# Kernel optimization log

Hardware: AMD Instinct MI355X
Metric: run time of the kernel (lower is better)

## Reference

```python
import jax, jax.numpy as jnp
import numpy as np

N = 50000       # nodes
E = 800000      # edges (before self loops)
F_IN = 128
NUM_CLASSES = 40
NEG_SLOPE = 0.2


def _glorot(key, shape):
    lim = jnp.sqrt(6.0 / (shape[0] + shape[1]))
    return jax.random.uniform(key, shape, jnp.float32, -lim, lim)


def setup_inputs() -> dict:
    key = jax.random.key(0)
    ks = jax.random.split(key, 32)
    inp = {}
    inp['x'] = jax.random.normal(ks[0], (N, F_IN), jnp.float32)
    inp['edge_index'] = jax.random.randint(ks[1], (2, E), 0, N, dtype=jnp.int32)
    dims = [(F_IN, 128), (128, 128), (128, 256)]
    k = 2
    for i, (din, dout) in enumerate(dims, start=1):
        inp[f'w{i}l'] = _glorot(ks[k], (din, dout)); k += 1
        inp[f'b{i}l'] = jnp.zeros((dout,), jnp.float32)
        inp[f'w{i}r'] = _glorot(ks[k], (din, dout)); k += 1
        inp[f'b{i}r'] = jnp.zeros((dout,), jnp.float32)
        inp[f'a{i}'] = _glorot(ks[k], (dout, 1))[:, 0]; k += 1
        inp[f'o{i}'] = jnp.zeros((dout,), jnp.float32)
    inp['wc'] = _glorot(ks[k], (256, NUM_CLASSES)); k += 1
    inp['bc'] = jnp.zeros((NUM_CLASSES,), jnp.float32)
    return inp


def gatv2_layer(x, src, dst, wl, bl, wr, br, att, bias, n):
    # GATv2 (heads=1): e_ij = att . leaky_relu(Wl x_j + Wr x_i); softmax over j per dst i
    xl = x @ wl + bl                     # [N, dout] (source transform)
    xr = x @ wr + br                     # [N, dout] (target transform)
    h = jax.nn.leaky_relu(xl[src] + xr[dst], NEG_SLOPE)   # [E, dout]
    e = h @ att                          # [E]
    m = jax.ops.segment_max(e, dst, num_segments=n)       # per-dst max (stable softmax)
    p = jnp.exp(e - m[dst])
    s = jax.ops.segment_sum(p, dst, num_segments=n)
    alpha = p / s[dst]                   # [E]
    out = jax.ops.segment_sum(alpha[:, None] * xl[src], dst, num_segments=n)
    return out + bias


def reference(x, edge_index,
              w1l, b1l, w1r, b1r, a1, o1,
              w2l, b2l, w2r, b2r, a2, o2,
              w3l, b3l, w3r, b3r, a3, o3,
              wc, bc):
    n = x.shape[0]
    loops = jnp.arange(n, dtype=edge_index.dtype)
    src = jnp.concatenate([edge_index[0], loops])   # add_self_loops=True (PyG default)
    dst = jnp.concatenate([edge_index[1], loops])
    h = gatv2_layer(x, src, dst, w1l, b1l, w1r, b1r, a1, o1, n)
    h = jax.nn.relu(h)                                # dropout inactive (eval mode)
    h = gatv2_layer(h, src, dst, w2l, b2l, w2r, b2r, a2, o2, n)
    h = jax.nn.relu(h)
    h = gatv2_layer(h, src, dst, w3l, b3l, w3r, b3r, a3, o3, n)
    return h @ wc + bc                                # [N, NUM_CLASSES]
```

## Files before the change

kernel.cpp:

```cpp
#include <hip/hip_runtime.h>
#include <math.h>
#include <stdint.h>


typedef __attribute__((ext_vector_type(8))) short bf16x8;
typedef __attribute__((ext_vector_type(4))) float f32x4;
typedef __attribute__((ext_vector_type(4))) _Float16 half4;
typedef __attribute__((ext_vector_type(2))) _Float16 half2v;
typedef unsigned short ushort_t;

__device__ inline ushort_t bf16_rne(float f) {
  unsigned u = __float_as_uint(f);
  unsigned r = (u + 0x7FFFu + ((u >> 16) & 1u)) >> 16;
  return (ushort_t)r;
}
__device__ inline float bf16_to_f(ushort_t h) {
  return __uint_as_float(((unsigned)h) << 16);
}

__device__ inline float fdot2f(half2v a, half2v b, float c) {
#if __has_builtin(__builtin_amdgcn_fdot2)
  return __builtin_amdgcn_fdot2(a, b, c, false);
#else
  return c + (float)a[0] * (float)b[0] + (float)a[1] * (float)b[1];
#endif
}
__device__ inline half2v h2max(half2v a, half2v b) {
#if __has_builtin(__builtin_elementwise_max)
  return __builtin_elementwise_max(a, b);
#else
  half2v r;
  r[0] = a[0] > b[0] ? a[0] : b[0];
  r[1] = a[1] > b[1] ? a[1] : b[1];
  return r;
#endif
}

__global__ void zero_int_kernel(int* __restrict__ p, int n) {
  int i = blockIdx.x * blockDim.x + threadIdx.x;
  if (i < n) p[i] = 0;
}

__global__ void deg_count_kernel(const int* __restrict__ dst, int E, int n,
                                 int* __restrict__ deg) {
  int i = blockIdx.x * blockDim.x + threadIdx.x;
  int tot = E + n;
  if (i < tot) {
    int d = (i < E) ? dst[i] : (i - E);
    atomicAdd(&deg[d], 1);
  }
}

__global__ __launch_bounds__(256) void block_sum_kernel(
    const int* __restrict__ deg, int n, int* __restrict__ partial) {
  __shared__ int sm[256];
  int base = blockIdx.x * 1024;
  int t = threadIdx.x;
  int sum = 0;
#pragma unroll
  for (int k = 0; k < 4; ++k) {
    int i = base + k * 256 + t;
    sum += (i < n) ? deg[i] : 0;
  }
  sm[t] = sum;
  __syncthreads();
  for (int off = 128; off > 0; off >>= 1) {
    if (t < off) sm[t] += sm[t + off];
    __syncthreads();
  }
  if (t == 0) partial[blockIdx.x] = sm[0];
}

__global__ void scan_partial_kernel(int* __restrict__ partial, int nchunks) {
  int lane = threadIdx.x;
  int v = (lane < nchunks) ? partial[lane] : 0;
#pragma unroll
  for (int off = 1; off < 64; off <<= 1) {
    int u = __shfl_up(v, off, 64);
    if (lane >= off) v += u;
  }
  int ex = __shfl_up(v, 1, 64);
  if (lane == 0) ex = 0;
  if (lane < nchunks) partial[lane] = ex;
}

__global__ __launch_bounds__(1024) void block_scan_kernel(
    const int* __restrict__ deg, const int* __restrict__ partial,
    int* __restrict__ row_ptr, int* __restrict__ cursor, int n) {
  __shared__ int sm[1024];
  int i = blockIdx.x * 1024 + threadIdx.x;
  int v = (i < n) ? deg[i] : 0;
  sm[threadIdx.x] = v;
  __syncthreads();
  for (int off = 1; off < 1024; off <<= 1) {
    int t = (threadIdx.x >= off) ? sm[threadIdx.x - off] : 0;
    __syncthreads();
    sm[threadIdx.x] += t;
    __syncthreads();
  }
  int excl = partial[blockIdx.x] + sm[threadIdx.x] - v;
  if (i < n) {
    row_ptr[i] = excl;
    cursor[i] = excl;
  }
  if (i == n - 1) row_ptr[n] = excl + v;
}

__global__ void scatter_kernel(const int* __restrict__ src,
                               const int* __restrict__ dst, int E, int n,
                               int* __restrict__ cursor,
                               int* __restrict__ col_src) {
  int i = blockIdx.x * blockDim.x + threadIdx.x;
  int tot = E + n;
  if (i < tot) {
    int s = (i < E) ? src[i] : (i - E);
    int d = (i < E) ? dst[i] : (i - E);
    int slot = atomicAdd(&cursor[d], 1);
    col_src[slot] = s;
  }
}

struct PackArgs {
  const float* w[7];
  ushort_t* hi[7];
  ushort_t* lo[7];
  int ntiles[7];
  int kslices[7];
  int N[7];
};

__global__ __launch_bounds__(256) void pack_w_kernel(PackArgs a) {
  int m = blockIdx.y;
  int ntiles = a.ntiles[m];
  int N = a.N[m];
  int tot = a.kslices[m] * ntiles * 512;
  int idx = blockIdx.x * 256 + threadIdx.x;
  if (idx >= tot) return;
  int i = idx & 7;
  int lane = (idx >> 3) & 63;
  int t = (idx >> 9) % ntiles;
  int ks = idx / (512 * ntiles);
  int k = ks * 32 + (lane >> 4) * 8 + i;
  int c = t * 16 + (lane & 15);
  float f = (c < N) ? a.w[m][k * N + c] : 0.f;
  ushort_t h = bf16_rne(f);
  a.hi[m][idx] = h;
  a.lo[m][idx] = bf16_rne(f - bf16_to_f(h));
}

__global__ __launch_bounds__(256) void gemm_dual_mfma(
    const float* __restrict__ X, const ushort_t* __restrict__ wlhi,
    const ushort_t* __restrict__ wllo, const ushort_t* __restrict__ wrhi,
    const ushort_t* __restrict__ wrlo, const float* __restrict__ Bl,
    const float* __restrict__ Br, _Float16* __restrict__ Yl,
    _Float16* __restrict__ Yr, int M, int N, int ntot) {
  int lane = threadIdx.x & 63;
  int wv = threadIdx.x >> 6;
  int kg = lane >> 4;
  int li = lane & 15;
  int rbase = blockIdx.x * 64 + wv * 16;
  int colofs = blockIdx.y * 128;
  int tbase = colofs >> 4;
  int arow = rbase + li;
  int ar = (arow < M) ? arow : (M - 1);
  const float* xp = X + (size_t)ar * 128 + kg * 8;

  f32x4 accl[8], accr[8];
#pragma unroll
  for (int t = 0; t < 8; ++t) {
    accl[t] = (f32x4){0.f, 0.f, 0.f, 0.f};
    accr[t] = (f32x4){0.f, 0.f, 0.f, 0.f};
  }

#pragma unroll
  for (int ks = 0; ks < 4; ++ks) {
    float4 a0 = *reinterpret_cast<const float4*>(xp + ks * 32);
    float4 a1 = *reinterpret_cast<const float4*>(xp + ks * 32 + 4);
    float av[8] = {a0.x, a0.y, a0.z, a0.w, a1.x, a1.y, a1.z, a1.w};
    bf16x8 ah, al;
#pragma unroll
    for (int i = 0; i < 8; ++i) {
      ushort_t h = bf16_rne(av[i]);
      ah[i] = (short)h;
      al[i] = (short)bf16_rne(av[i] - bf16_to_f(h));
    }
    size_t fb = ((size_t)ks * ntot + tbase) * 512 + (size_t)lane * 8;
#pragma unroll
    for (int t = 0; t < 8; ++t) {
      size_t o = fb + (size_t)t * 512;
      bf16x8 blh = *reinterpret_cast<const bf16x8*>(wlhi + o);
      bf16x8 bll = *reinterpret_cast<const bf16x8*>(wllo + o);
      bf16x8 brh = *reinterpret_cast<const bf16x8*>(wrhi + o);
      bf16x8 brl = *reinterpret_cast<const bf16x8*>(wrlo + o);
      accl[t] = __builtin_amdgcn_mfma_f32_16x16x32_bf16(ah, blh, accl[t], 0, 0, 0);
      accl[t] = __builtin_amdgcn_mfma_f32_16x16x32_bf16(ah, bll, accl[t], 0, 0, 0);
      accl[t] = __builtin_amdgcn_mfma_f32_16x16x32_bf16(al, blh, accl[t], 0, 0, 0);
      accr[t] = __builtin_amdgcn_mfma_f32_16x16x32_bf16(ah, brh, accr[t], 0, 0, 0);
      accr[t] = __builtin_amdgcn_mfma_f32_16x16x32_bf16(ah, brl, accr[t], 0, 0, 0);
      accr[t] = __builtin_amdgcn_mfma_f32_16x16x32_bf16(al, brh, accr[t], 0, 0, 0);
    }
  }
  int srow = rbase + kg * 4;
#pragma unroll
  for (int t = 0; t < 8; ++t) {
    int col = colofs + t * 16 + li;
    float bl = Bl[col];
    float br = Br[col];
#pragma unroll
    for (int r = 0; r < 4; ++r) {
      int rr = srow + r;
      if (rr < M) {
        Yl[(size_t)rr * N + col] = (_Float16)(accl[t][r] + bl);
        Yr[(size_t)rr * N + col] = (_Float16)(accr[t][r] + br);
      }
    }
  }
}

__global__ __launch_bounds__(256) void classifier_mfma(
    const float* __restrict__ H, const ushort_t* __restrict__ wchi,
    const ushort_t* __restrict__ wclo, const float* __restrict__ BC,
    float* __restrict__ out, int M) {
  int lane = threadIdx.x & 63;
  int wv = threadIdx.x >> 6;
  int kg = lane >> 4;
  int li = lane & 15;
  int rbase = blockIdx.x * 64 + wv * 16;
  int arow = rbase + li;
  int ar = (arow < M) ? arow : (M - 1);
  const float* xp = H + (size_t)ar * 256 + kg * 8;

  f32x4 acc[3];
#pragma unroll
  for (int t = 0; t < 3; ++t) acc[t] = (f32x4){0.f, 0.f, 0.f, 0.f};

#pragma unroll
  for (int ks = 0; ks < 8; ++ks) {
    float4 a0 = *reinterpret_cast<const float4*>(xp + ks * 32);
    float4 a1 = *reinterpret_cast<const float4*>(xp + ks * 32 + 4);
    float av[8] = {a0.x, a0.y, a0.z, a0.w, a1.x, a1.y, a1.z, a1.w};
    bf16x8 ah, al;
#pragma unroll
    for (int i = 0; i < 8; ++i) {
      ushort_t h = bf16_rne(av[i]);
      ah[i] = (short)h;
      al[i] = (short)bf16_rne(av[i] - bf16_to_f(h));
    }
    size_t fb = ((size_t)ks * 3) * 512 + (size_t)lane * 8;
#pragma unroll
    for (int t = 0; t < 3; ++t) {
      size_t o = fb + (size_t)t * 512;
      bf16x8 bh = *reinterpret_cast<const bf16x8*>(wchi + o);
      bf16x8 bl = *reinterpret_cast<const bf16x8*>(wclo + o);
      acc[t] = __builtin_amdgcn_mfma_f32_16x16x32_bf16(ah, bh, acc[t], 0, 0, 0);
      acc[t] = __builtin_amdgcn_mfma_f32_16x16x32_bf16(ah, bl, acc[t], 0, 0, 0);
      acc[t] = __builtin_amdgcn_mfma_f32_16x16x32_bf16(al, bh, acc[t], 0, 0, 0);
    }
  }
  int srow = rbase + kg * 4;
#pragma unroll
  for (int t = 0; t < 3; ++t) {
    int col = t * 16 + li;
    if (col < 40) {
      float b = BC[col];
#pragma unroll
      for (int r = 0; r < 4; ++r) {
        int rr = srow + r;
        if (rr < M) out[(size_t)rr * 40 + col] = acc[t][r] + b;
      }
    }
  }
}

#define NEG_BIG (-1e30f)
template <int DOUT, bool RELU>
__global__ __launch_bounds__(256) void attn_kernel(
    const _Float16* __restrict__ xl, const _Float16* __restrict__ xr,
    const float* __restrict__ att, const float* __restrict__ bias,
    const int* __restrict__ row_ptr, const int* __restrict__ col_src,
    float* __restrict__ out, int M) {
  constexpr int NQ = DOUT / 64;
  constexpr int NE = NQ * 4;
  int wid = (int)((blockIdx.x * blockDim.x + threadIdx.x) >> 6);
  int lane = threadIdx.x & 63;
  int grp = lane >> 4;
  int sl = lane & 15;
  if (wid >= M) return;

  half2v xr2[NQ * 2], att2[NQ * 2];
  {
    const half4* xrp =
        reinterpret_cast<const half4*>(xr) + (size_t)wid * (DOUT / 4) + sl;
#pragma unroll
    for (int q = 0; q < NQ; ++q) {
      half4 r4 = xrp[q * 16];
      half2v lo, hi;
      lo[0] = r4[0]; lo[1] = r4[1];
      hi[0] = r4[2]; hi[1] = r4[3];
      xr2[q * 2] = lo;
      xr2[q * 2 + 1] = hi;
    }
#pragma unroll
    for (int q = 0; q < NQ; ++q) {
#pragma unroll
      for (int t = 0; t < 2; ++t) {
        int c = q * 64 + sl * 4 + t * 2;
        half2v a2;
        a2[0] = (_Float16)att[c];
        a2[1] = (_Float16)att[c + 1];
        att2[q * 2 + t] = a2;
      }
    }
  }
  half2v v02;
  v02[0] = (_Float16)0.2f;
  v02[1] = (_Float16)0.2f;

  float acc[NE];
#pragma unroll
  for (int i = 0; i < NE; ++i) acc[i] = 0.f;
  float m = NEG_BIG, s = 0.f;
  int e0 = row_ptr[wid], e1 = row_ptr[wid + 1];
  int j = e0 + grp;

  const half4* base = reinterpret_cast<const half4*>(xl);
  half4 xv[NQ], xn[NQ], x2[NQ];
  half4 hz;
  hz[0] = hz[1] = hz[2] = hz[3] = (_Float16)0.f;
#pragma unroll
  for (int q = 0; q < NQ; ++q) {
    xv[q] = hz;
    xn[q] = hz;
    x2[q] = hz;
  }
  if (j < e1) {
    const half4* rp = base + (size_t)col_src[j] * (DOUT / 4) + sl;
#pragma unroll
    for (int q = 0; q < NQ; ++q) xv[q] = rp[q * 16];
  }
  if (j + 4 < e1) {
    const half4* rp = base + (size_t)col_src[j + 4] * (DOUT / 4) + sl;
#pragma unroll
    for (int q = 0; q < NQ; ++q) xn[q] = rp[q * 16];
  }
  int i2 = (j + 8 < e1) ? col_src[j + 8] : 0;

  while (j < e1) {
    int i3 = (j + 12 < e1) ? col_src[j + 12] : 0;
    if (j + 8 < e1) {
      const half4* rp = base + (size_t)i2 * (DOUT / 4) + sl;
#pragma unroll
      for (int q = 0; q < NQ; ++q) x2[q] = rp[q * 16];
    }
    float p = 0.f;
    float xf[NE];
#pragma unroll
    for (int q = 0; q < NQ; ++q) {
#pragma unroll
      for (int t = 0; t < 2; ++t) {
        half2v xa;
        xa[0] = xv[q][2 * t];
        xa[1] = xv[q][2 * t + 1];
        half2v tt = xa + xr2[q * 2 + t];
        tt = h2max(tt, tt * v02);
        p = fdot2f(tt, att2[q * 2 + t], p);
        xf[q * 4 + 2 * t] = (float)xa[0];
        xf[q * 4 + 2 * t + 1] = (float)xa[1];
      }
    }
#pragma unroll
    for (int off = 1; off < 16; off <<= 1) p += __shfl_xor(p, off, 64);
    if (p > m + 8.0f) {
      float sc = __expf(m - p);
      s = s * sc + 1.f;
#pragma unroll
      for (int i = 0; i < NE; ++i) acc[i] = fmaf(acc[i], sc, xf[i]);
      m = p;
    } else {
      float pe = __expf(p - m);
      s += pe;
#pragma unroll
      for (int i = 0; i < NE; ++i) acc[i] = fmaf(pe, xf[i], acc[i]);
    }
#pragma unroll
    for (int q = 0; q < NQ; ++q) {
      xv[q] = xn[q];
      xn[q] = x2[q];
    }
    i2 = i3;
    j += 4;
  }
  float mg = m;
  float mm = m, ss = s;
#pragma unroll
  for (int off = 16; off < 64; off <<= 1) {
    float mo = __shfl_xor(mm, off, 64);
    float so = __shfl_xor(ss, off, 64);
    float nm = fmaxf(mm, mo);
    ss = ss * __expf(mm - nm) + so * __expf(mo - nm);
    mm = nm;
  }
  float scale = __expf(mg - mm) / ss;
#pragma unroll
  for (int i = 0; i < NE; ++i) {
    float v = acc[i] * scale;
#pragma unroll
    for (int off = 16; off < 64; off <<= 1) v += __shfl_xor(v, off, 64);
    acc[i] = v;
  }
#pragma unroll
  for (int q = 0; q < NQ; ++q) {
    if (grp == (q & 3)) {
      int c = q * 64 + sl * 4;
      float4 b4 = *reinterpret_cast<const float4*>(bias + c);
      float4 o;
      o.x = acc[q * 4 + 0] + b4.x;
      o.y = acc[q * 4 + 1] + b4.y;
      o.z = acc[q * 4 + 2] + b4.z;
      o.w = acc[q * 4 + 3] + b4.w;
      if (RELU) {
        o.x = fmaxf(o.x, 0.f); o.y = fmaxf(o.y, 0.f);
        o.z = fmaxf(o.z, 0.f); o.w = fmaxf(o.w, 0.f);
      }
      *reinterpret_cast<float4*>(out + (size_t)wid * DOUT + c) = o;
    }
  }
}

extern "C" void kernel_launch(void* const* d_in, const int* in_sizes, int n_in,
                              void* d_out, int out_size, void* d_ws,
                              size_t ws_size, hipStream_t stream) {
  const float* x = (const float*)d_in[0];
  const int* ei = (const int*)d_in[1];
  const float* w1l = (const float*)d_in[2];
  const float* b1l = (const float*)d_in[3];
  const float* w1r = (const float*)d_in[4];
  const float* b1r = (const float*)d_in[5];
  const float* a1 = (const float*)d_in[6];
  const float* o1 = (const float*)d_in[7];
  const float* w2l = (const float*)d_in[8];
  const float* b2l = (const float*)d_in[9];
  const float* w2r = (const float*)d_in[10];
  const float* b2r = (const float*)d_in[11];
  const float* a2 = (const float*)d_in[12];
  const float* o2 = (const float*)d_in[13];
  const float* w3l = (const float*)d_in[14];
  const float* b3l = (const float*)d_in[15];
  const float* w3r = (const float*)d_in[16];
  const float* b3r = (const float*)d_in[17];
  const float* a3 = (const float*)d_in[18];
  const float* o3 = (const float*)d_in[19];
  const float* wc = (const float*)d_in[20];
  const float* bc = (const float*)d_in[21];
  float* out = (float*)d_out;

  const int n = in_sizes[0] / 128;
  const int E = in_sizes[1] / 2;
  const int tot = E + n;
  const int nchunks = (n + 1023) / 1024;

  char* p = (char*)d_ws;
  int* row_ptr = (int*)p; p += (size_t)(n + 1) * 4;
  int* deg = (int*)p;     p += (size_t)n * 4;
  int* cursor = (int*)p;  p += (size_t)n * 4;
  int* partial = (int*)p; p += (size_t)64 * 4;
  int* col_src = (int*)p; p += (size_t)tot * 4;
  p = (char*)(((uintptr_t)p + 255) & ~(uintptr_t)255);
  const size_t SZ12 = 16384, SZ3 = 32768, SZC = 12288;
  ushort_t* pk[14];
  for (int i = 0; i < 8; ++i) { pk[i] = (ushort_t*)p; p += SZ12 * 2; }
  for (int i = 8; i < 12; ++i) { pk[i] = (ushort_t*)p; p += SZ3 * 2; }
  for (int i = 12; i < 14; ++i) { pk[i] = (ushort_t*)p; p += SZC * 2; }
  p = (char*)(((uintptr_t)p + 255) & ~(uintptr_t)255);
  float* bufA = (float*)p;       p += (size_t)n * 256 * 4;
  _Float16* bufL = (_Float16*)p; p += (size_t)n * 256 * 2;
  _Float16* bufR = (_Float16*)p;

  const int TPB = 256;

  zero_int_kernel<<<(n + TPB - 1) / TPB, TPB, 0, stream>>>(deg, n);
  deg_count_kernel<<<(tot + TPB - 1) / TPB, TPB, 0, stream>>>(ei + E, E, n, deg);
  block_sum_kernel<<<nchunks, 256, 0, stream>>>(deg, n, partial);
  scan_partial_kernel<<<1, 64, 0, stream>>>(partial, nchunks);
  block_scan_kernel<<<nchunks, 1024, 0, stream>>>(deg, partial, row_ptr, cursor, n);
  scatter_kernel<<<(tot + TPB - 1) / TPB, TPB, 0, stream>>>(ei, ei + E, E, n,
                                                            cursor, col_src);

  PackArgs pa;
  pa.w[0] = w1l; pa.w[1] = w1r; pa.w[2] = w2l; pa.w[3] = w2r;
  pa.w[4] = w3l; pa.w[5] = w3r; pa.w[6] = wc;
  pa.hi[0] = pk[0]; pa.lo[0] = pk[1];
  pa.hi[1] = pk[2]; pa.lo[1] = pk[3];
  pa.hi[2] = pk[4]; pa.lo[2] = pk[5];
  pa.hi[3] = pk[6]; pa.lo[3] = pk[7];
  pa.hi[4] = pk[8]; pa.lo[4] = pk[9];
  pa.hi[5] = pk[10]; pa.lo[5] = pk[11];
  pa.hi[6] = pk[12]; pa.lo[6] = pk[13];
  pa.ntiles[0] = pa.ntiles[1] = pa.ntiles[2] = pa.ntiles[3] = 8;
  pa.ntiles[4] = pa.ntiles[5] = 16;
  pa.ntiles[6] = 3;
  pa.kslices[0] = pa.kslices[1] = pa.kslices[2] = pa.kslices[3] = 4;
  pa.kslices[4] = pa.kslices[5] = 4;
  pa.kslices[6] = 8;
  pa.N[0] = pa.N[1] = pa.N[2] = pa.N[3] = 128;
  pa.N[4] = pa.N[5] = 256;
  pa.N[6] = 40;
  pack_w_kernel<<<dim3(128, 7), 256, 0, stream>>>(pa);

  const int gemmGrid = (n + 63) / 64;
  const int waveGrid = (n + 3) / 4;

  gemm_dual_mfma<<<dim3(gemmGrid, 1), TPB, 0, stream>>>(
      x, pk[0], pk[1], pk[2], pk[3], b1l, b1r, bufL, bufR, n, 128, 8);
  attn_kernel<128, true><<<waveGrid, TPB, 0, stream>>>(bufL, bufR, a1, o1,
                                                       row_ptr, col_src, bufA, n);
  gemm_dual_mfma<<<dim3(gemmGrid, 1), TPB, 0, stream>>>(
      bufA, pk[4], pk[5], pk[6], pk[7], b2l, b2r, bufL, bufR, n, 128, 8);
  attn_kernel<128, true><<<waveGrid, TPB, 0, stream>>>(bufL, bufR, a2, o2,
                                                       row_ptr, col_src, bufA, n);
  gemm_dual_mfma<<<dim3(gemmGrid, 2), TPB, 0, stream>>>(
      bufA, pk[8], pk[9], pk[10], pk[11], b3l, b3r, bufL, bufR, n, 256, 16);
  attn_kernel<256, false><<<waveGrid, TPB, 0, stream>>>(bufL, bufR, a3, o3,
                                                        row_ptr, col_src, bufA, n);
  classifier_mfma<<<gemmGrid, TPB, 0, stream>>>(bufA, pk[12], pk[13], bc, out, n);
}
```

Before: 433.9 us.

## Store attention outputs in fp16 and unroll gather pipeline into rotating register sets

The attention kernel now writes its per-node output in half precision, and the following GEMMs and the classifier read fp16 activations instead of fp32. This halves activation traffic between layers. The gather loop is also restructured: three register buffers are processed in rotation by an unrolled macro, which removes the per-iteration register shuffling of the prefetch pipeline. The cost is extra fp16 rounding of intermediate activations, which may affect accuracy.

```diff
diff --git a/kernel.cpp b/kernel.cpp
--- a/kernel.cpp
+++ b/kernel.cpp
@@ -6,6 +6,7 @@
 typedef __attribute__((ext_vector_type(8))) short bf16x8;
 typedef __attribute__((ext_vector_type(4))) float f32x4;
 typedef __attribute__((ext_vector_type(4))) _Float16 half4;
+typedef __attribute__((ext_vector_type(8))) _Float16 half8;
 typedef __attribute__((ext_vector_type(2))) _Float16 half2v;
 typedef unsigned short ushort_t;
 
@@ -148,8 +149,9 @@
   a.lo[m][idx] = bf16_rne(f - bf16_to_f(h));
 }
 
+template <typename TIN>
 __global__ __launch_bounds__(256) void gemm_dual_mfma(
-    const float* __restrict__ X, const ushort_t* __restrict__ wlhi,
+    const TIN* __restrict__ X, const ushort_t* __restrict__ wlhi,
     const ushort_t* __restrict__ wllo, const ushort_t* __restrict__ wrhi,
     const ushort_t* __restrict__ wrlo, const float* __restrict__ Bl,
     const float* __restrict__ Br, _Float16* __restrict__ Yl,
@@ -163,7 +165,7 @@
   int tbase = colofs >> 4;
   int arow = rbase + li;
   int ar = (arow < M) ? arow : (M - 1);
-  const float* xp = X + (size_t)ar * 128 + kg * 8;
+  const TIN* xp = X + (size_t)ar * 128 + kg * 8;
 
   f32x4 accl[8], accr[8];
 #pragma unroll
@@ -174,9 +176,17 @@
 
 #pragma unroll
   for (int ks = 0; ks < 4; ++ks) {
-    float4 a0 = *reinterpret_cast<const float4*>(xp + ks * 32);
-    float4 a1 = *reinterpret_cast<const float4*>(xp + ks * 32 + 4);
-    float av[8] = {a0.x, a0.y, a0.z, a0.w, a1.x, a1.y, a1.z, a1.w};
+    float av[8];
+    if constexpr (sizeof(TIN) == 4) {
+      float4 a0 = *reinterpret_cast<const float4*>(xp + ks * 32);
+      float4 a1 = *reinterpret_cast<const float4*>(xp + ks * 32 + 4);
+      av[0] = a0.x; av[1] = a0.y; av[2] = a0.z; av[3] = a0.w;
+      av[4] = a1.x; av[5] = a1.y; av[6] = a1.z; av[7] = a1.w;
+    } else {
+      half8 h8 = *reinterpret_cast<const half8*>(xp + ks * 32);
+#pragma unroll
+      for (int i = 0; i < 8; ++i) av[i] = (float)h8[i];
+    }
     bf16x8 ah, al;
 #pragma unroll
     for (int i = 0; i < 8; ++i) {
@@ -218,7 +228,7 @@
 }
 
 __global__ __launch_bounds__(256) void classifier_mfma(
-    const float* __restrict__ H, const ushort_t* __restrict__ wchi,
+    const _Float16* __restrict__ H, const ushort_t* __restrict__ wchi,
     const ushort_t* __restrict__ wclo, const float* __restrict__ BC,
     float* __restrict__ out, int M) {
   int lane = threadIdx.x & 63;
@@ -228,7 +238,7 @@
   int rbase = blockIdx.x * 64 + wv * 16;
   int arow = rbase + li;
   int ar = (arow < M) ? arow : (M - 1);
-  const float* xp = H + (size_t)ar * 256 + kg * 8;
+  const _Float16* xp = H + (size_t)ar * 256 + kg * 8;
 
   f32x4 acc[3];
 #pragma unroll
@@ -236,15 +246,14 @@
 
 #pragma unroll
   for (int ks = 0; ks < 8; ++ks) {
-    float4 a0 = *reinterpret_cast<const float4*>(xp + ks * 32);
-    float4 a1 = *reinterpret_cast<const float4*>(xp + ks * 32 + 4);
-    float av[8] = {a0.x, a0.y, a0.z, a0.w, a1.x, a1.y, a1.z, a1.w};
+    half8 h8 = *reinterpret_cast<const half8*>(xp + ks * 32);
     bf16x8 ah, al;
 #pragma unroll
     for (int i = 0; i < 8; ++i) {
-      ushort_t h = bf16_rne(av[i]);
+      float f = (float)h8[i];
+      ushort_t h = bf16_rne(f);
       ah[i] = (short)h;
-      al[i] = (short)bf16_rne(av[i] - bf16_to_f(h));
+      al[i] = (short)bf16_rne(f - bf16_to_f(h));
     }
     size_t fb = ((size_t)ks * 3) * 512 + (size_t)lane * 8;
 #pragma unroll
@@ -273,12 +282,50 @@
 }
 
 #define NEG_BIG (-1e30f)
+
+#define PROC3(X)                                                          \
+  {                                                                       \
+    int inx = (j + 12 < e1) ? col_src[j + 12] : 0;                        \
+    float p = 0.f;                                                        \
+    float xf[NE];                                                         \
+    _Pragma("unroll") for (int q = 0; q < NQ; ++q) {                      \
+      _Pragma("unroll") for (int t = 0; t < 2; ++t) {                     \
+        half2v xa;                                                        \
+        xa[0] = X[q][2 * t];                                              \
+        xa[1] = X[q][2 * t + 1];                                          \
+        half2v tt = xa + xr2[q * 2 + t];                                  \
+        tt = h2max(tt, tt * v02);                                         \
+        p = fdot2f(tt, att2[q * 2 + t], p);                               \
+        xf[q * 4 + 2 * t] = (float)xa[0];                                 \
+        xf[q * 4 + 2 * t + 1] = (float)xa[1];                             \
+      }                                                                   \
+    }                                                                     \
+    {                                                                     \
+      const half4* rp = base + (size_t)inx * (DOUT / 4) + sl;             \
+      _Pragma("unroll") for (int q = 0; q < NQ; ++q) X[q] = rp[q * 16];   \
+    }                                                                     \
+    _Pragma("unroll") for (int off = 1; off < 16; off <<= 1)              \
+        p += __shfl_xor(p, off, 64);                                      \
+    if (p > m + 8.0f) {                                                   \
+      float sc = __expf(m - p);                                           \
+      s = s * sc + 1.f;                                                   \
+      _Pragma("unroll") for (int i = 0; i < NE; ++i)                      \
+          acc[i] = fmaf(acc[i], sc, xf[i]);                               \
+      m = p;                                                              \
+    } else {                                                              \
+      float pe = __expf(p - m);                                           \
+      s += pe;                                                            \
+      _Pragma("unroll") for (int i = 0; i < NE; ++i)                      \
+          acc[i] = fmaf(pe, xf[i], acc[i]);                               \
+    }                                                                     \
+  }
+
 template <int DOUT, bool RELU>
 __global__ __launch_bounds__(256) void attn_kernel(
     const _Float16* __restrict__ xl, const _Float16* __restrict__ xr,
     const float* __restrict__ att, const float* __restrict__ bias,
     const int* __restrict__ row_ptr, const int* __restrict__ col_src,
-    float* __restrict__ out, int M) {
+    _Float16* __restrict__ out, int M) {
   constexpr int NQ = DOUT / 64;
   constexpr int NE = NQ * 4;
   int wid = (int)((blockIdx.x * blockDim.x + threadIdx.x) >> 6);
@@ -324,72 +371,33 @@
   int j = e0 + grp;
 
   const half4* base = reinterpret_cast<const half4*>(xl);
-  half4 xv[NQ], xn[NQ], x2[NQ];
-  half4 hz;
-  hz[0] = hz[1] = hz[2] = hz[3] = (_Float16)0.f;
-#pragma unroll
-  for (int q = 0; q < NQ; ++q) {
-    xv[q] = hz;
-    xn[q] = hz;
-    x2[q] = hz;
-  }
-  if (j < e1) {
-    const half4* rp = base + (size_t)col_src[j] * (DOUT / 4) + sl;
-#pragma unroll
-    for (int q = 0; q < NQ; ++q) xv[q] = rp[q * 16];
-  }
-  if (j + 4 < e1) {
-    const half4* rp = base + (size_t)col_src[j + 4] * (DOUT / 4) + sl;
-#pragma unroll
-    for (int q = 0; q < NQ; ++q) xn[q] = rp[q * 16];
-  }
-  int i2 = (j + 8 < e1) ? col_src[j + 8] : 0;
+  half4 Axv[NQ], Bxv[NQ], Cxv[NQ];
+  {
+    int iA = (j < e1) ? col_src[j] : 0;
+    int iB = (j + 4 < e1) ? col_src[j + 4] : 0;
+    int iC = (j + 8 < e1) ? col_src[j + 8] : 0;
+    const half4* rpA = base + (size_t)iA * (DOUT / 4) + sl;
+    const half4* rpB = base + (size_t)iB * (DOUT / 4) + sl;
+    const half4* rpC = base + (size_t)iC * (DOUT / 4) + sl;
+#pragma unroll
+    for (int q = 0; q < NQ; ++q) Axv[q] = rpA[q * 16];
+#pragma unroll
+    for (int q = 0; q < NQ; ++q) Bxv[q] = rpB[q * 16];
+#pragma unroll
+    for (int q = 0; q < NQ; ++q) Cxv[q] = rpC[q * 16];
+  }
 
   while (j < e1) {
-    int i3 = (j + 12 < e1) ? col_src[j + 12] : 0;
-    if (j + 8 < e1) {
-      const half4* rp = base + (size_t)i2 * (DOUT / 4) + sl;
-#pragma unroll
-      for (int q = 0; q < NQ; ++q) x2[q] = rp[q * 16];
-    }
-    float p = 0.f;
-    float xf[NE];
-#pragma unroll
-    for (int q = 0; q < NQ; ++q) {
-#pragma unroll
-      for (int t = 0; t < 2; ++t) {
-        half2v xa;
-        xa[0] = xv[q][2 * t];
-        xa[1] = xv[q][2 * t + 1];
-        half2v tt = xa + xr2[q * 2 + t];
-        tt = h2max(tt, tt * v02);
-        p = fdot2f(tt, att2[q * 2 + t], p);
-        xf[q * 4 + 2 * t] = (float)xa[0];
-        xf[q * 4 + 2 * t + 1] = (float)xa[1];
-      }
-    }
-#pragma unroll
-    for (int off = 1; off < 16; off <<= 1) p += __shfl_xor(p, off, 64);
-    if (p > m + 8.0f) {
-      float sc = __expf(m - p);
-      s = s * sc + 1.f;
-#pragma unroll
-      for (int i = 0; i < NE; ++i) acc[i] = fmaf(acc[i], sc, xf[i]);
-      m = p;
-    } else {
-      float pe = __expf(p - m);
-      s += pe;
-#pragma unroll
-      for (int i = 0; i < NE; ++i) acc[i] = fmaf(pe, xf[i], acc[i]);
-    }
-#pragma unroll
-    for (int q = 0; q < NQ; ++q) {
-      xv[q] = xn[q];
-      xn[q] = x2[q];
-    }
-    i2 = i3;
+    PROC3(Axv);
     j += 4;
-  }
+    if (j >= e1) break;
+    PROC3(Bxv);
+    j += 4;
+    if (j >= e1) break;
+    PROC3(Cxv);
+    j += 4;
+  }
+
   float mg = m;
   float mm = m, ss = s;
 #pragma unroll
@@ -413,16 +421,18 @@
     if (grp == (q & 3)) {
       int c = q * 64 + sl * 4;
       float4 b4 = *reinterpret_cast<const float4*>(bias + c);
-      float4 o;
-      o.x = acc[q * 4 + 0] + b4.x;
-      o.y = acc[q * 4 + 1] + b4.y;
-      o.z = acc[q * 4 + 2] + b4.z;
-      o.w = acc[q * 4 + 3] + b4.w;
+      float o0 = acc[q * 4 + 0] + b4.x;
+      float o1 = acc[q * 4 + 1] + b4.y;
+      float o2 = acc[q * 4 + 2] + b4.z;
+      float o3 = acc[q * 4 + 3] + b4.w;
       if (RELU) {
-        o.x = fmaxf(o.x, 0.f); o.y = fmaxf(o.y, 0.f);
-        o.z = fmaxf(o.z, 0.f); o.w = fmaxf(o.w, 0.f);
+        o0 = fmaxf(o0, 0.f); o1 = fmaxf(o1, 0.f);
+        o2 = fmaxf(o2, 0.f); o3 = fmaxf(o3, 0.f);
       }
-      *reinterpret_cast<float4*>(out + (size_t)wid * DOUT + c) = o;
+      half4 oh;
+      oh[0] = (_Float16)o0; oh[1] = (_Float16)o1;
+      oh[2] = (_Float16)o2; oh[3] = (_Float16)o3;
+      *reinterpret_cast<half4*>(out + (size_t)wid * DOUT + c) = oh;
     }
   }
 }
@@ -472,7 +482,7 @@
   for (int i = 8; i < 12; ++i) { pk[i] = (ushort_t*)p; p += SZ3 * 2; }
   for (int i = 12; i < 14; ++i) { pk[i] = (ushort_t*)p; p += SZC * 2; }
   p = (char*)(((uintptr_t)p + 255) & ~(uintptr_t)255);
-  float* bufA = (float*)p;       p += (size_t)n * 256 * 4;
+  _Float16* bufA = (_Float16*)p; p += (size_t)n * 256 * 2;
   _Float16* bufL = (_Float16*)p; p += (size_t)n * 256 * 2;
   _Float16* bufR = (_Float16*)p;
 
@@ -510,15 +520,15 @@
   const int gemmGrid = (n + 63) / 64;
   const int waveGrid = (n + 3) / 4;
 
-  gemm_dual_mfma<<<dim3(gemmGrid, 1), TPB, 0, stream>>>(
+  gemm_dual_mfma<float><<<dim3(gemmGrid, 1), TPB, 0, stream>>>(
       x, pk[0], pk[1], pk[2], pk[3], b1l, b1r, bufL, bufR, n, 128, 8);
   attn_kernel<128, true><<<waveGrid, TPB, 0, stream>>>(bufL, bufR, a1, o1,
                                                        row_ptr, col_src, bufA, n);
-  gemm_dual_mfma<<<dim3(gemmGrid, 1), TPB, 0, stream>>>(
+  gemm_dual_mfma<_Float16><<<dim3(gemmGrid, 1), TPB, 0, stream>>>(
       bufA, pk[4], pk[5], pk[6], pk[7], b2l, b2r, bufL, bufR, n, 128, 8);
   attn_kernel<128, true><<<waveGrid, TPB, 0, stream>>>(bufL, bufR, a2, o2,
                                                        row_ptr, col_src, bufA, n);
-  gemm_dual_mfma<<<dim3(gemmGrid, 2), TPB, 0, stream>>>(
+  gemm_dual_mfma<_Float16><<<dim3(gemmGrid, 2), TPB, 0, stream>>>(
       bufA, pk[8], pk[9], pk[10], pk[11], b3l, b3r, bufL, bufR, n, 256, 16);
   attn_kernel<256, false><<<waveGrid, TPB, 0, stream>>>(bufL, bufR, a3, o3,
                                                         row_ptr, col_src, bufA, n);
```

New measurement: 407.1 us. 6.2% less time.

## Store attention outputs in fp16 and widen gathers to 16-byte half8 loads

Applied to the files above, without the earlier changes.

The attention kernel now writes its per-node output as fp16 instead of fp32, and the following GEMMs and classifier read fp16 activations. This halves the bytes written and re-read between layers. The attention gather also switches from half4 to half8 vector loads, so each lane covers 8 features and fetches 16 bytes per neighbor row. The risks are fp16 rounding of post-ReLU activations, which could cost accuracy, and a different output-lane mapping that leaves half the groups idle on the store in the 128-wide layers.

```diff
diff --git a/kernel.cpp b/kernel.cpp
--- a/kernel.cpp
+++ b/kernel.cpp
@@ -6,6 +6,7 @@
 typedef __attribute__((ext_vector_type(8))) short bf16x8;
 typedef __attribute__((ext_vector_type(4))) float f32x4;
 typedef __attribute__((ext_vector_type(4))) _Float16 half4;
+typedef __attribute__((ext_vector_type(8))) _Float16 half8;
 typedef __attribute__((ext_vector_type(2))) _Float16 half2v;
 typedef unsigned short ushort_t;
 
@@ -148,8 +149,9 @@
   a.lo[m][idx] = bf16_rne(f - bf16_to_f(h));
 }
 
+template <typename TIN>
 __global__ __launch_bounds__(256) void gemm_dual_mfma(
-    const float* __restrict__ X, const ushort_t* __restrict__ wlhi,
+    const TIN* __restrict__ X, const ushort_t* __restrict__ wlhi,
     const ushort_t* __restrict__ wllo, const ushort_t* __restrict__ wrhi,
     const ushort_t* __restrict__ wrlo, const float* __restrict__ Bl,
     const float* __restrict__ Br, _Float16* __restrict__ Yl,
@@ -163,7 +165,7 @@
   int tbase = colofs >> 4;
   int arow = rbase + li;
   int ar = (arow < M) ? arow : (M - 1);
-  const float* xp = X + (size_t)ar * 128 + kg * 8;
+  const TIN* xp = X + (size_t)ar * 128 + kg * 8;
 
   f32x4 accl[8], accr[8];
 #pragma unroll
@@ -174,9 +176,17 @@
 
 #pragma unroll
   for (int ks = 0; ks < 4; ++ks) {
-    float4 a0 = *reinterpret_cast<const float4*>(xp + ks * 32);
-    float4 a1 = *reinterpret_cast<const float4*>(xp + ks * 32 + 4);
-    float av[8] = {a0.x, a0.y, a0.z, a0.w, a1.x, a1.y, a1.z, a1.w};
+    float av[8];
+    if constexpr (sizeof(TIN) == 4) {
+      float4 a0 = *reinterpret_cast<const float4*>(xp + ks * 32);
+      float4 a1 = *reinterpret_cast<const float4*>(xp + ks * 32 + 4);
+      av[0] = a0.x; av[1] = a0.y; av[2] = a0.z; av[3] = a0.w;
+      av[4] = a1.x; av[5] = a1.y; av[6] = a1.z; av[7] = a1.w;
+    } else {
+      half8 h8 = *reinterpret_cast<const half8*>(xp + ks * 32);
+#pragma unroll
+      for (int i = 0; i < 8; ++i) av[i] = (float)h8[i];
+    }
     bf16x8 ah, al;
 #pragma unroll
     for (int i = 0; i < 8; ++i) {
@@ -218,7 +228,7 @@
 }
 
 __global__ __launch_bounds__(256) void classifier_mfma(
-    const float* __restrict__ H, const ushort_t* __restrict__ wchi,
+    const _Float16* __restrict__ H, const ushort_t* __restrict__ wchi,
     const ushort_t* __restrict__ wclo, const float* __restrict__ BC,
     float* __restrict__ out, int M) {
   int lane = threadIdx.x & 63;
@@ -228,7 +238,7 @@
   int rbase = blockIdx.x * 64 + wv * 16;
   int arow = rbase + li;
   int ar = (arow < M) ? arow : (M - 1);
-  const float* xp = H + (size_t)ar * 256 + kg * 8;
+  const _Float16* xp = H + (size_t)ar * 256 + kg * 8;
 
   f32x4 acc[3];
 #pragma unroll
@@ -236,15 +246,14 @@
 
 #pragma unroll
   for (int ks = 0; ks < 8; ++ks) {
-    float4 a0 = *reinterpret_cast<const float4*>(xp + ks * 32);
-    float4 a1 = *reinterpret_cast<const float4*>(xp + ks * 32 + 4);
-    float av[8] = {a0.x, a0.y, a0.z, a0.w, a1.x, a1.y, a1.z, a1.w};
+    half8 h8 = *reinterpret_cast<const half8*>(xp + ks * 32);
     bf16x8 ah, al;
 #pragma unroll
     for (int i = 0; i < 8; ++i) {
-      ushort_t h = bf16_rne(av[i]);
+      float f = (float)h8[i];
+      ushort_t h = bf16_rne(f);
       ah[i] = (short)h;
-      al[i] = (short)bf16_rne(av[i] - bf16_to_f(h));
+      al[i] = (short)bf16_rne(f - bf16_to_f(h));
     }
     size_t fb = ((size_t)ks * 3) * 512 + (size_t)lane * 8;
 #pragma unroll
@@ -278,37 +287,40 @@
     const _Float16* __restrict__ xl, const _Float16* __restrict__ xr,
     const float* __restrict__ att, const float* __restrict__ bias,
     const int* __restrict__ row_ptr, const int* __restrict__ col_src,
-    float* __restrict__ out, int M) {
-  constexpr int NQ = DOUT / 64;
-  constexpr int NE = NQ * 4;
+    _Float16* __restrict__ out, int M) {
+  constexpr int NQ8 = DOUT / 128;
+  constexpr int NE = DOUT / 16;
+  constexpr int NP = NE / 2;
   int wid = (int)((blockIdx.x * blockDim.x + threadIdx.x) >> 6);
   int lane = threadIdx.x & 63;
   int grp = lane >> 4;
   int sl = lane & 15;
   if (wid >= M) return;
 
-  half2v xr2[NQ * 2], att2[NQ * 2];
+  half2v xr2[NP], att2[NP];
   {
-    const half4* xrp =
-        reinterpret_cast<const half4*>(xr) + (size_t)wid * (DOUT / 4) + sl;
-#pragma unroll
-    for (int q = 0; q < NQ; ++q) {
-      half4 r4 = xrp[q * 16];
-      half2v lo, hi;
-      lo[0] = r4[0]; lo[1] = r4[1];
-      hi[0] = r4[2]; hi[1] = r4[3];
-      xr2[q * 2] = lo;
-      xr2[q * 2 + 1] = hi;
-    }
-#pragma unroll
-    for (int q = 0; q < NQ; ++q) {
-#pragma unroll
-      for (int t = 0; t < 2; ++t) {
-        int c = q * 64 + sl * 4 + t * 2;
+    const half8* xrp =
+        reinterpret_cast<const half8*>(xr) + (size_t)wid * (DOUT / 8) + sl;
+#pragma unroll
+    for (int q = 0; q < NQ8; ++q) {
+      half8 r8 = xrp[q * 16];
+#pragma unroll
+      for (int t = 0; t < 4; ++t) {
+        half2v v;
+        v[0] = r8[2 * t];
+        v[1] = r8[2 * t + 1];
+        xr2[q * 4 + t] = v;
+      }
+    }
+#pragma unroll
+    for (int q = 0; q < NQ8; ++q) {
+#pragma unroll
+      for (int t = 0; t < 4; ++t) {
+        int c = q * 128 + sl * 8 + t * 2;
         half2v a2;
         a2[0] = (_Float16)att[c];
         a2[1] = (_Float16)att[c + 1];
-        att2[q * 2 + t] = a2;
+        att2[q * 4 + t] = a2;
       }
     }
   }
@@ -323,49 +335,50 @@
   int e0 = row_ptr[wid], e1 = row_ptr[wid + 1];
   int j = e0 + grp;
 
-  const half4* base = reinterpret_cast<const half4*>(xl);
-  half4 xv[NQ], xn[NQ], x2[NQ];
-  half4 hz;
-  hz[0] = hz[1] = hz[2] = hz[3] = (_Float16)0.f;
-#pragma unroll
-  for (int q = 0; q < NQ; ++q) {
+  const half8* base = reinterpret_cast<const half8*>(xl);
+  half8 xv[NQ8], xn[NQ8], x2[NQ8];
+  half8 hz;
+#pragma unroll
+  for (int i = 0; i < 8; ++i) hz[i] = (_Float16)0.f;
+#pragma unroll
+  for (int q = 0; q < NQ8; ++q) {
     xv[q] = hz;
     xn[q] = hz;
     x2[q] = hz;
   }
   if (j < e1) {
-    const half4* rp = base + (size_t)col_src[j] * (DOUT / 4) + sl;
-#pragma unroll
-    for (int q = 0; q < NQ; ++q) xv[q] = rp[q * 16];
+    const half8* rp = base + (size_t)col_src[j] * (DOUT / 8) + sl;
+#pragma unroll
+    for (int q = 0; q < NQ8; ++q) xv[q] = rp[q * 16];
   }
   if (j + 4 < e1) {
-    const half4* rp = base + (size_t)col_src[j + 4] * (DOUT / 4) + sl;
-#pragma unroll
-    for (int q = 0; q < NQ; ++q) xn[q] = rp[q * 16];
+    const half8* rp = base + (size_t)col_src[j + 4] * (DOUT / 8) + sl;
+#pragma unroll
+    for (int q = 0; q < NQ8; ++q) xn[q] = rp[q * 16];
   }
   int i2 = (j + 8 < e1) ? col_src[j + 8] : 0;
 
   while (j < e1) {
     int i3 = (j + 12 < e1) ? col_src[j + 12] : 0;
     if (j + 8 < e1) {
-      const half4* rp = base + (size_t)i2 * (DOUT / 4) + sl;
-#pragma unroll
-      for (int q = 0; q < NQ; ++q) x2[q] = rp[q * 16];
+      const half8* rp = base + (size_t)i2 * (DOUT / 8) + sl;
+#pragma unroll
+      for (int q = 0; q < NQ8; ++q) x2[q] = rp[q * 16];
     }
     float p = 0.f;
     float xf[NE];
 #pragma unroll
-    for (int q = 0; q < NQ; ++q) {
-#pragma unroll
-      for (int t = 0; t < 2; ++t) {
+    for (int q = 0; q < NQ8; ++q) {
+#pragma unroll
+      for (int t = 0; t < 4; ++t) {
         half2v xa;
         xa[0] = xv[q][2 * t];
         xa[1] = xv[q][2 * t + 1];
-        half2v tt = xa + xr2[q * 2 + t];
+        half2v tt = xa + xr2[q * 4 + t];
         tt = h2max(tt, tt * v02);
-        p = fdot2f(tt, att2[q * 2 + t], p);
-        xf[q * 4 + 2 * t] = (float)xa[0];
-        xf[q * 4 + 2 * t + 1] = (float)xa[1];
+        p = fdot2f(tt, att2[q * 4 + t], p);
+        xf[q * 8 + 2 * t] = (float)xa[0];
+        xf[q * 8 + 2 * t + 1] = (float)xa[1];
       }
     }
 #pragma unroll
@@ -383,7 +396,7 @@
       for (int i = 0; i < NE; ++i) acc[i] = fmaf(pe, xf[i], acc[i]);
     }
 #pragma unroll
-    for (int q = 0; q < NQ; ++q) {
+    for (int q = 0; q < NQ8; ++q) {
       xv[q] = xn[q];
       xn[q] = x2[q];
     }
@@ -408,22 +421,39 @@
     for (int off = 16; off < 64; off <<= 1) v += __shfl_xor(v, off, 64);
     acc[i] = v;
   }
-#pragma unroll
-  for (int q = 0; q < NQ; ++q) {
-    if (grp == (q & 3)) {
-      int c = q * 64 + sl * 4;
+  if (NQ8 == 1) {
+    if (grp < 2) {
+      int c = sl * 8 + grp * 4;
       float4 b4 = *reinterpret_cast<const float4*>(bias + c);
-      float4 o;
-      o.x = acc[q * 4 + 0] + b4.x;
-      o.y = acc[q * 4 + 1] + b4.y;
-      o.z = acc[q * 4 + 2] + b4.z;
-      o.w = acc[q * 4 + 3] + b4.w;
+      float o0 = acc[grp * 4 + 0] + b4.x;
+      float o1 = acc[grp * 4 + 1] + b4.y;
+      float o2 = acc[grp * 4 + 2] + b4.z;
+      float o3 = acc[grp * 4 + 3] + b4.w;
       if (RELU) {
-        o.x = fmaxf(o.x, 0.f); o.y = fmaxf(o.y, 0.f);
-        o.z = fmaxf(o.z, 0.f); o.w = fmaxf(o.w, 0.f);
+        o0 = fmaxf(o0, 0.f); o1 = fmaxf(o1, 0.f);
+        o2 = fmaxf(o2, 0.f); o3 = fmaxf(o3, 0.f);
       }
-      *reinterpret_cast<float4*>(out + (size_t)wid * DOUT + c) = o;
-    }
+      half4 oh;
+      oh[0] = (_Float16)o0; oh[1] = (_Float16)o1;
+      oh[2] = (_Float16)o2; oh[3] = (_Float16)o3;
+      *reinterpret_cast<half4*>(out + (size_t)wid * DOUT + c) = oh;
+    }
+  } else {
+    int q8 = grp >> 1, hf = grp & 1;
+    int c = q8 * 128 + sl * 8 + hf * 4;
+    float4 b4 = *reinterpret_cast<const float4*>(bias + c);
+    float o0 = acc[q8 * 8 + hf * 4 + 0] + b4.x;
+    float o1 = acc[q8 * 8 + hf * 4 + 1] + b4.y;
+    float o2 = acc[q8 * 8 + hf * 4 + 2] + b4.z;
+    float o3 = acc[q8 * 8 + hf * 4 + 3] + b4.w;
+    if (RELU) {
+      o0 = fmaxf(o0, 0.f); o1 = fmaxf(o1, 0.f);
+      o2 = fmaxf(o2, 0.f); o3 = fmaxf(o3, 0.f);
+    }
+    half4 oh;
+    oh[0] = (_Float16)o0; oh[1] = (_Float16)o1;
+    oh[2] = (_Float16)o2; oh[3] = (_Float16)o3;
+    *reinterpret_cast<half4*>(out + (size_t)wid * DOUT + c) = oh;
   }
 }
 
@@ -472,7 +502,7 @@
   for (int i = 8; i < 12; ++i) { pk[i] = (ushort_t*)p; p += SZ3 * 2; }
   for (int i = 12; i < 14; ++i) { pk[i] = (ushort_t*)p; p += SZC * 2; }
   p = (char*)(((uintptr_t)p + 255) & ~(uintptr_t)255);
-  float* bufA = (float*)p;       p += (size_t)n * 256 * 4;
+  _Float16* bufA = (_Float16*)p; p += (size_t)n * 256 * 2;
   _Float16* bufL = (_Float16*)p; p += (size_t)n * 256 * 2;
   _Float16* bufR = (_Float16*)p;
 
@@ -510,15 +540,15 @@
   const int gemmGrid = (n + 63) / 64;
   const int waveGrid = (n + 3) / 4;
 
-  gemm_dual_mfma<<<dim3(gemmGrid, 1), TPB, 0, stream>>>(
+  gemm_dual_mfma<float><<<dim3(gemmGrid, 1), TPB, 0, stream>>>(
       x, pk[0], pk[1], pk[2], pk[3], b1l, b1r, bufL, bufR, n, 128, 8);
   attn_kernel<128, true><<<waveGrid, TPB, 0, stream>>>(bufL, bufR, a1, o1,
                                                        row_ptr, col_src, bufA, n);
-  gemm_dual_mfma<<<dim3(gemmGrid, 1), TPB, 0, stream>>>(
+  gemm_dual_mfma<_Float16><<<dim3(gemmGrid, 1), TPB, 0, stream>>>(
       bufA, pk[4], pk[5], pk[6], pk[7], b2l, b2r, bufL, bufR, n, 128, 8);
   attn_kernel<128, true><<<waveGrid, TPB, 0, stream>>>(bufL, bufR, a2, o2,
                                                        row_ptr, col_src, bufA, n);
-  gemm_dual_mfma<<<dim3(gemmGrid, 2), TPB, 0, stream>>>(
+  gemm_dual_mfma<_Float16><<<dim3(gemmGrid, 2), TPB, 0, stream>>>(
       bufA, pk[8], pk[9], pk[10], pk[11], b3l, b3r, bufL, bufR, n, 256, 16);
   attn_kernel<256, false><<<waveGrid, TPB, 0, stream>>>(bufL, bufR, a3, o3,
                                                         row_ptr, col_src, bufA, n);
```

After: 411.8 us. 5.1% less time.
